# Performance work log

Measured on AMD Instinct MI355X. Metric: run time of the kernel, lower is better.

The kernel has to match this reference:

```python
import jax, jax.numpy as jnp
import numpy as np

B, L, H, NH, D, I = 2, 2048, 2048, 16, 128, 8192
EPS = 1e-6
ROPE_BASE = 10000.0


def rms_norm(x, w):
    x32 = x.astype(jnp.float32)
    n = x32 * jax.lax.rsqrt(jnp.mean(x32 * x32, axis=-1, keepdims=True) + EPS)
    return (n * w).astype(x.dtype)


def rope(x, offset):
    # x: [B, L, H, D], non-traditional (half-split) RoPE
    d = x.shape[-1]
    half = d // 2
    inv_freq = 1.0 / (ROPE_BASE ** (jnp.arange(half, dtype=jnp.float32) * 2.0 / d))
    pos = jnp.arange(x.shape[1], dtype=jnp.float32) + offset
    ang = pos[:, None] * inv_freq[None, :]              # [L, half]
    cos = jnp.cos(ang)[None, :, None, :]
    sin = jnp.sin(ang)[None, :, None, :]
    x1, x2 = x[..., :half], x[..., half:]
    out = jnp.concatenate([x1 * cos - x2 * sin, x2 * cos + x1 * sin], axis=-1)
    return out.astype(x.dtype)


def setup_inputs() -> dict:
    key = jax.random.key(0)
    ks = jax.random.split(key, 9)
    s = 0.02
    causal = jnp.where(jnp.tril(jnp.ones((L, L), dtype=bool)), 0.0, -1e9).astype(jnp.float32)
    return {
        "x": jax.random.normal(ks[0], (B, L, H), dtype=jnp.float32),
        "ln1_w": jnp.ones((H,), dtype=jnp.float32),
        "ln2_w": jnp.ones((H,), dtype=jnp.float32),
        "wq": jax.random.normal(ks[1], (H, H), dtype=jnp.float32) * s,
        "wk": jax.random.normal(ks[2], (H, H), dtype=jnp.float32) * s,
        "wv": jax.random.normal(ks[3], (H, H), dtype=jnp.float32) * s,
        "wo": jax.random.normal(ks[4], (H, H), dtype=jnp.float32) * s,
        "w_gate": jax.random.normal(ks[5], (I, H), dtype=jnp.float32) * s,
        "w_up": jax.random.normal(ks[6], (I, H), dtype=jnp.float32) * s,
        "w_down": jax.random.normal(ks[7], (H, I), dtype=jnp.float32) * s,
        "mask": causal,
        "offset": 0,
    }


def reference(x, ln1_w, ln2_w, wq, wk, wv, wo, w_gate, w_up, w_down, mask, offset):
    residual = x
    h = rms_norm(x, ln1_w)
    # QKV projections (torch Linear: y = x @ W.T)
    q = jnp.einsum("ble,oe->blo", h, wq).reshape(B, L, NH, D)
    k = jnp.einsum("ble,oe->blo", h, wk).reshape(B, L, NH, D)
    v = jnp.einsum("ble,oe->blo", h, wv).reshape(B, L, NH, D)
    q = rope(q, offset)
    k = rope(k, offset)
    # [B, NH, L, D]
    q = q.transpose(0, 2, 1, 3)
    k = k.transpose(0, 2, 1, 3)
    v = v.transpose(0, 2, 1, 3)
    scores = jnp.einsum("bhqd,bhkd->bhqk", q.astype(jnp.float32), k.astype(jnp.float32))
    scores = scores / np.sqrt(D).astype(np.float32)
    if mask is not None:
        scores = scores + mask
    probs = jax.nn.softmax(scores, axis=-1).astype(v.dtype)
    attn = jnp.einsum("bhqk,bhkd->bhqd", probs, v)
    attn = attn.transpose(0, 2, 1, 3).reshape(B, L, NH * D)
    h = jnp.einsum("blo,eo->ble", attn, wo)
    x = h + residual
    residual = x
    h = rms_norm(x, ln2_w)
    gate = jax.nn.silu(jnp.einsum("ble,ie->bli", h, w_gate))
    up = jnp.einsum("ble,ie->bli", h, w_up)
    mlp = jnp.einsum("bli,ei->ble", gate * up, w_down)
    return mlp + residual
```

## Files before the change

### kernel.cpp

```cpp
#include <hip/hip_runtime.h>
#include <stdint.h>

#define B_ 2
#define L_ 2048
#define H_ 2048
#define NH_ 16
#define D_ 128
#define I_ 8192
#define M_ (B_*L_)

typedef unsigned short u16;
typedef __attribute__((ext_vector_type(8))) short bf16x8;
typedef __attribute__((ext_vector_type(4))) float f32x4;

__device__ __forceinline__ u16 f2bf(float f) {
  union { float f; uint32_t u; } c; c.f = f;
  return (u16)((c.u + 0x7fffu + ((c.u >> 16) & 1u)) >> 16);
}
__device__ __forceinline__ float bf2f(u16 h) {
  union { uint32_t u; float f; } c; c.u = ((uint32_t)h) << 16;
  return c.f;
}
__device__ __forceinline__ void gload16(const void* g, void* l) {
  __builtin_amdgcn_global_load_lds(
      (__attribute__((address_space(1))) void*)g,
      (__attribute__((address_space(3))) void*)l, 16, 0, 0);
}

__global__ void cvt_w(const float* __restrict__ src, u16* __restrict__ dst, int n4) {
  int i = blockIdx.x * blockDim.x + threadIdx.x;
  if (i >= n4) return;
  float4 v = ((const float4*)src)[i];
  ushort4 o;
  o.x = f2bf(v.x); o.y = f2bf(v.y); o.z = f2bf(v.z); o.w = f2bf(v.w);
  ((ushort4*)dst)[i] = o;
}

__global__ __launch_bounds__(256) void down_reduce(const u16* __restrict__ p0,
                                                   const u16* __restrict__ p1,
                                                   const float* __restrict__ res,
                                                   float* __restrict__ out, int n4) {
  int i = blockIdx.x * blockDim.x + threadIdx.x;
  if (i >= n4) return;
  ushort4 a = ((const ushort4*)p0)[i];
  ushort4 b = ((const ushort4*)p1)[i];
  float4 r = ((const float4*)res)[i];
  float4 o;
  o.x = bf2f(a.x) + bf2f(b.x) + r.x;
  o.y = bf2f(a.y) + bf2f(b.y) + r.y;
  o.z = bf2f(a.z) + bf2f(b.z) + r.z;
  o.w = bf2f(a.w) + bf2f(b.w) + r.w;
  ((float4*)out)[i] = o;
}

__global__ __launch_bounds__(256) void rmsnorm_k(const float* __restrict__ x,
                                                 const float* __restrict__ w,
                                                 u16* __restrict__ out) {
  int row = blockIdx.x;
  int t = threadIdx.x;
  const float4* xr = (const float4*)(x + (size_t)row * H_);
  float4 a = xr[t * 2], b = xr[t * 2 + 1];
  float s = a.x*a.x + a.y*a.y + a.z*a.z + a.w*a.w
          + b.x*b.x + b.y*b.y + b.z*b.z + b.w*b.w;
  for (int m = 1; m < 64; m <<= 1) s += __shfl_xor(s, m);
  __shared__ float sm[4];
  if ((t & 63) == 0) sm[t >> 6] = s;
  __syncthreads();
  float tot = sm[0] + sm[1] + sm[2] + sm[3];
  float rs = rsqrtf(tot / (float)H_ + 1e-6f);
  const float4* wr = (const float4*)w;
  float4 w0 = wr[t * 2], w1 = wr[t * 2 + 1];
  ushort4 o0, o1;
  o0.x = f2bf(a.x * rs * w0.x); o0.y = f2bf(a.y * rs * w0.y);
  o0.z = f2bf(a.z * rs * w0.z); o0.w = f2bf(a.w * rs * w0.w);
  o1.x = f2bf(b.x * rs * w1.x); o1.y = f2bf(b.y * rs * w1.y);
  o1.z = f2bf(b.z * rs * w1.z); o1.w = f2bf(b.w * rs * w1.w);
  ushort4* orow = (ushort4*)(out + (size_t)row * H_);
  orow[t * 2] = o0; orow[t * 2 + 1] = o1;
}

__global__ void rope_tab(float* __restrict__ cosT, float* __restrict__ sinT,
                         const int* __restrict__ offp) {
  int i = blockIdx.x * blockDim.x + threadIdx.x;
  int d = i & 63, l = i >> 6;
  float inv = powf(10000.0f, -(float)d / 64.0f);
  float ang = (float)(l + *offp) * inv;
  cosT[i] = cosf(ang);
  sinT[i] = sinf(ang);
}

__global__ void rope_apply(u16* __restrict__ qk, const float* __restrict__ cosT,
                           const float* __restrict__ sinT) {
  int i = blockIdx.x * blockDim.x + threadIdx.x;
  int d = i & 63;
  size_t row = (size_t)(i >> 6);
  int l = (int)(row & (L_ - 1));
  u16* p = qk + row * D_;
  float x1 = bf2f(p[d]), x2 = bf2f(p[d + 64]);
  float c = cosT[l * 64 + d], s = sinT[l * 64 + d];
  p[d]      = f2bf(x1 * c - x2 * s);
  p[d + 64] = f2bf(x2 * c + x1 * s);
}

__global__ __launch_bounds__(256) void vtrans_k(const u16* __restrict__ v,
                                                u16* __restrict__ vt) {
  __shared__ u16 tile[64][65];
  int l0 = blockIdx.x * 64, d0 = blockIdx.y * 64;
  size_t base = (size_t)blockIdx.z * L_ * D_;
  int t = threadIdx.x;
  int tr = t >> 3, tc = (t & 7) * 8;
  #pragma unroll
  for (int it = 0; it < 2; ++it) {
    int r = tr + it * 32;
    const u16* src = v + base + (size_t)(l0 + r) * D_ + d0 + tc;
    ushort4 u0 = ((const ushort4*)src)[0], u1 = ((const ushort4*)src)[1];
    tile[r][tc + 0] = u0.x; tile[r][tc + 1] = u0.y;
    tile[r][tc + 2] = u0.z; tile[r][tc + 3] = u0.w;
    tile[r][tc + 4] = u1.x; tile[r][tc + 5] = u1.y;
    tile[r][tc + 6] = u1.z; tile[r][tc + 7] = u1.w;
  }
  __syncthreads();
  #pragma unroll
  for (int it = 0; it < 2; ++it) {
    int r = tr + it * 32;
    u16* dst = vt + base + (size_t)(d0 + r) * L_ + l0 + tc;
    ushort4 o0, o1;
    o0.x = tile[tc + 0][r]; o0.y = tile[tc + 1][r];
    o0.z = tile[tc + 2][r]; o0.w = tile[tc + 3][r];
    o1.x = tile[tc + 4][r]; o1.y = tile[tc + 5][r];
    o1.z = tile[tc + 6][r]; o1.w = tile[tc + 7][r];
    ((ushort4*)dst)[0] = o0; ((ushort4*)dst)[1] = o1;
  }
}

#define EPI_SILU 1
#define EPI_MUL 2
#define EPI_PART 4
#define EPI_QKV3 5

template <int EPI>
__global__ __launch_bounds__(512, 2)
void gemm256(const u16* __restrict__ A, const u16* __restrict__ Bw,
             int M, int N, int K, int nk,
             u16* __restrict__ outb, u16* __restrict__ outb2) {
  __shared__ __attribute__((aligned(16))) u16 Asm[2][2][8192];
  __shared__ __attribute__((aligned(16))) u16 Bsm[2][2][8192];
  int tid = threadIdx.x;
  int wid = tid >> 6, lane = tid & 63;
  int r16 = lane & 15, g4 = lane >> 4;
  int nwg = gridDim.x, bid = blockIdx.x;
  int q8 = nwg >> 3, r8 = nwg & 7, xcd = bid & 7, loc = bid >> 3;
  int wgall = (xcd < r8 ? xcd * (q8 + 1) : r8 * (q8 + 1) + (xcd - r8) * q8) + loc;
  int nwg_geo = (M >> 8) * (N >> 8);
  int ks = wgall / nwg_geo;
  int wg = wgall % nwg_geo;
  int MX = M >> 8;
  int m0 = (wg % MX) * 256;
  int n0 = (wg / MX) * 256;
  const char* Ab = (const char*)(A + (size_t)ks * nk * 64);
  const char* Bb = (const char*)(Bw + (size_t)ks * nk * 64);
  u16* ob = (EPI == EPI_PART && ks) ? outb2 : outb;

  f32x4 acc[2][2][4][2] = {};
  bf16x8 afr[4][2];
  bf16x8 bfr[2][2][2];

  auto STAGE = [&](int kt1, int sel) {
    if (kt1 >= nk) return;
    int buf = kt1 & 1;
    int k0 = kt1 << 6;
    const char* gb; char* lb; int row0;
    if (sel == 0)      { gb = Ab; row0 = m0;       lb = (char*)&Asm[buf][0][0]; }
    else if (sel == 3) { gb = Ab; row0 = m0 + 128; lb = (char*)&Asm[buf][1][0]; }
    else if (sel == 1) { gb = Bb; row0 = n0;       lb = (char*)&Bsm[buf][0][0]; }
    else               { gb = Bb; row0 = n0 + 128; lb = (char*)&Bsm[buf][1][0]; }
    #pragma unroll
    for (int j = 0; j < 2; ++j) {
      int p = j * 8192 + wid * 1024 + lane * 16;
      int r = p >> 7;
      int cb = (p & 127) ^ ((r & 7) << 4);
      gload16(gb + ((size_t)(row0 + r) * K + k0) * 2 + cb,
              lb + j * 8192 + wid * 1024);
    }
  };

  STAGE(0, 0); STAGE(0, 1); STAGE(0, 2); STAGE(0, 3);

  const int QM[4] = {0, 0, 1, 1};
  const int QN[4] = {0, 1, 1, 0};

  for (int kt = 0; kt < nk; ++kt) {
    int cur = kt & 1;
    #pragma unroll
    for (int ph = 0; ph < 4; ++ph) {
      if (ph < 3) {
        __builtin_amdgcn_sched_barrier(0);
        asm volatile("s_waitcnt vmcnt(4)" ::: "memory");
      }
      __builtin_amdgcn_s_barrier();
      __builtin_amdgcn_sched_barrier(0);
      const int qm = QM[ph], qn = QN[ph];
      if (ph == 0 || ph == 2) {
        const char* Ah = (const char*)&Asm[cur][qm][0];
        #pragma unroll
        for (int mf = 0; mf < 4; ++mf) {
          int R = (wid >> 2) * 64 + mf * 16 + r16;
          int sw = (R & 7) << 4;
          afr[mf][0] = *(const bf16x8*)(Ah + R * 128 + ((g4 * 16) ^ sw));
          afr[mf][1] = *(const bf16x8*)(Ah + R * 128 + ((64 + g4 * 16) ^ sw));
        }
      }
      if (ph == 0 || ph == 1) {
        const char* Bh = (const char*)&Bsm[cur][qn][0];
        #pragma unroll
        for (int nf = 0; nf < 2; ++nf) {
          int R = (wid & 3) * 32 + nf * 16 + r16;
          int sw = (R & 7) << 4;
          bfr[qn][nf][0] = *(const bf16x8*)(Bh + R * 128 + ((g4 * 16) ^ sw));
          bfr[qn][nf][1] = *(const bf16x8*)(Bh + R * 128 + ((64 + g4 * 16) ^ sw));
        }
      }
      STAGE(kt + 1, ph);
      __builtin_amdgcn_s_setprio(1);
      #pragma unroll
      for (int mf = 0; mf < 4; ++mf)
        #pragma unroll
        for (int nf = 0; nf < 2; ++nf)
          #pragma unroll
          for (int kk = 0; kk < 2; ++kk)
            acc[qm][qn][mf][nf] = __builtin_amdgcn_mfma_f32_16x16x32_bf16(
                afr[mf][kk], bfr[qn][nf][kk], acc[qm][qn][mf][nf], 0, 0, 0);
      __builtin_amdgcn_s_setprio(0);
    }
  }
  #pragma unroll
  for (int qm = 0; qm < 2; ++qm)
    #pragma unroll
    for (int qn = 0; qn < 2; ++qn)
      #pragma unroll
      for (int mf = 0; mf < 4; ++mf)
        #pragma unroll
        for (int nf = 0; nf < 2; ++nf)
          #pragma unroll
          for (int rr = 0; rr < 4; ++rr) {
            int row = m0 + qm * 128 + (wid >> 2) * 64 + mf * 16 + g4 * 4 + rr;
            int col = n0 + qn * 128 + (wid & 3) * 32 + nf * 16 + r16;
            float val = acc[qm][qn][mf][nf][rr];
            if (EPI == EPI_SILU) {
              ob[(size_t)row * N + col] = f2bf(val / (1.0f + __expf(-val)));
            } else if (EPI == EPI_MUL) {
              float g = bf2f(ob[(size_t)row * N + col]);
              ob[(size_t)row * N + col] = f2bf(g * val);
            } else if (EPI == EPI_PART) {
              ob[(size_t)row * N + col] = f2bf(val);
            } else if (EPI == EPI_QKV3) {
              int which = col >> 11, within = col & 2047;
              int hh = within >> 7, d = within & 127;
              int bb = row >> 11, l = row & 2047;
              ob[(size_t)which * M_ * H_ +
                 ((((size_t)bb * NH_ + hh) * L_ + l) << 7) + d] = f2bf(val);
            }
          }
}

__global__ __launch_bounds__(256)
void flash_attn(const u16* __restrict__ q, const u16* __restrict__ k,
                const u16* __restrict__ vt, u16* __restrict__ out) {
  __shared__ __attribute__((aligned(16))) u16 Kt[2][64 * 128];
  __shared__ __attribute__((aligned(16))) u16 Vt[2][128 * 64];
  __shared__ __attribute__((aligned(16))) u16 Pl[4][16 * 64];
  int tid = threadIdx.x, w = tid >> 6, lane = tid & 63;
  int r16 = lane & 15, g4 = lane >> 4;
  int b = blockIdx.z, h = blockIdx.y;
  int qt = gridDim.x - 1 - blockIdx.x;
  int q0 = qt * 64;
  size_t bh = (size_t)b * NH_ + h;
  const char* qb = (const char*)(q + bh * L_ * D_);
  const char* kb = (const char*)(k + bh * L_ * D_);
  const char* vb = (const char*)(vt + bh * D_ * L_);
  int qrow = q0 + w * 16 + r16;
  bf16x8 qf[4];
  #pragma unroll
  for (int c = 0; c < 4; ++c)
    qf[c] = *(const bf16x8*)(qb + ((size_t)qrow * 128 + c * 32 + g4 * 8) * 2);
  f32x4 oacc[8] = {};
  float mrow[4], lsum[4];
  #pragma unroll
  for (int r = 0; r < 4; ++r) { mrow[r] = -3.0e38f; lsum[r] = 0.f; }
  int myq = q0 + w * 16 + g4 * 4;
  int ntiles = qt + 1;
  int rsw = (r16 & 7) << 4;
  const float sc = 0.08838834764831845f;

  auto STAGEKV = [&](int t, int buf) {
    if (t >= ntiles) return;
    int kv0 = t * 64;
    #pragma unroll
    for (int i = 0; i < 4; ++i) {
      int uoff = i * 4096 + w * 1024;
      int lin = uoff + lane * 16;
      int krow = lin >> 8;
      int kcol = (lin & 255) ^ ((krow & 7) << 4);
      gload16(kb + (size_t)(kv0 + krow) * 256 + kcol,
              (char*)&Kt[buf][0] + uoff);
      int vrow = lin >> 7;
      int vcol = (lin & 127) ^ ((vrow & 7) << 4);
      gload16(vb + (size_t)vrow * (L_ * 2) + kv0 * 2 + vcol,
              (char*)&Vt[buf][0] + uoff);
    }
  };

  STAGEKV(0, 0);
  __syncthreads();

  for (int t = 0; t < ntiles; ++t) {
    int buf = t & 1;
    int kv0 = t * 64;
    STAGEKV(t + 1, buf ^ 1);
    const char* Kb = (const char*)&Kt[buf][0];
    const char* Vb = (const char*)&Vt[buf][0];
    f32x4 s[4] = {};
    __builtin_amdgcn_s_setprio(1);
    #pragma unroll
    for (int c = 0; c < 4; ++c) {
      #pragma unroll
      for (int n = 0; n < 4; ++n) {
        bf16x8 kf = *(const bf16x8*)(Kb + (n * 16 + r16) * 256
                                     + ((c * 64 + g4 * 16) ^ rsw));
        s[n] = __builtin_amdgcn_mfma_f32_16x16x32_bf16(qf[c], kf, s[n], 0, 0, 0);
      }
    }
    __builtin_amdgcn_s_setprio(0);
    #pragma unroll
    for (int r = 0; r < 4; ++r) {
      float rm = -3.0e38f;
      #pragma unroll
      for (int n = 0; n < 4; ++n) {
        float v = s[n][r] * sc;
        int kvi = kv0 + n * 16 + r16;
        if (kvi > myq + r) v = -3.0e38f;
        s[n][r] = v;
        rm = fmaxf(rm, v);
      }
      rm = fmaxf(rm, __shfl_xor(rm, 1));
      rm = fmaxf(rm, __shfl_xor(rm, 2));
      rm = fmaxf(rm, __shfl_xor(rm, 4));
      rm = fmaxf(rm, __shfl_xor(rm, 8));
      float mnew = fmaxf(mrow[r], rm);
      float alpha = __expf(mrow[r] - mnew);
      mrow[r] = mnew;
      lsum[r] *= alpha;
      #pragma unroll
      for (int nf = 0; nf < 8; ++nf) oacc[nf][r] *= alpha;
      int prow = g4 * 4 + r;
      int psw = (prow & 7) << 3;
      #pragma unroll
      for (int n = 0; n < 4; ++n) {
        float pv = __expf(s[n][r] - mnew);
        lsum[r] += pv;
        Pl[w][prow * 64 + ((n * 16 + r16) ^ psw)] = f2bf(pv);
      }
    }
    asm volatile("s_waitcnt lgkmcnt(0)" ::: "memory");
    __builtin_amdgcn_sched_barrier(0);
    __builtin_amdgcn_s_setprio(1);
    #pragma unroll
    for (int kc = 0; kc < 2; ++kc) {
      bf16x8 pf = *(const bf16x8*)((const char*)&Pl[w][0] + r16 * 128
                                   + ((kc * 64 + g4 * 16) ^ rsw));
      #pragma unroll
      for (int nf = 0; nf < 8; ++nf) {
        bf16x8 vf = *(const bf16x8*)(Vb + (nf * 16 + r16) * 128
                                     + ((kc * 64 + g4 * 16) ^ rsw));
        oacc[nf] = __builtin_amdgcn_mfma_f32_16x16x32_bf16(pf, vf, oacc[nf], 0, 0, 0);
      }
    }
    __builtin_amdgcn_s_setprio(0);
    __syncthreads();
  }
  #pragma unroll
  for (int r = 0; r < 4; ++r) {
    float l = lsum[r];
    l += __shfl_xor(l, 1); l += __shfl_xor(l, 2);
    l += __shfl_xor(l, 4); l += __shfl_xor(l, 8);
    float inv = 1.0f / l;
    size_t orow = ((size_t)b * L_ + (myq + r)) * H_ + h * D_;
    #pragma unroll
    for (int nf = 0; nf < 8; ++nf)
      out[orow + nf * 16 + r16] = f2bf(oacc[nf][r] * inv);
  }
}

extern "C" void kernel_launch(void* const* d_in, const int* in_sizes, int n_in,
                              void* d_out, int out_size, void* d_ws, size_t ws_size,
                              hipStream_t stream) {
  (void)in_sizes; (void)n_in; (void)out_size; (void)ws_size;
  const float* x    = (const float*)d_in[0];
  const float* ln1w = (const float*)d_in[1];
  const float* ln2w = (const float*)d_in[2];
  const float* wq   = (const float*)d_in[3];
  const float* wk   = (const float*)d_in[4];
  const float* wv   = (const float*)d_in[5];
  const float* wo   = (const float*)d_in[6];
  const float* wg   = (const float*)d_in[7];
  const float* wu   = (const float*)d_in[8];
  const float* wd   = (const float*)d_in[9];
  const int*   offp = (const int*)d_in[11];
  float* out = (float*)d_out;

  char* p = (char*)d_ws;
  auto alloc = [&](size_t bytes) {
    char* r = p;
    p += (bytes + 255) & ~(size_t)255;
    return r;
  };
  const size_t HH = (size_t)H_ * H_, IH = (size_t)I_ * H_;
  u16* wbuf = (u16*)alloc(IH * 2);
  u16* h1   = (u16*)alloc((size_t)M_ * H_ * 2);
  u16* qb   = (u16*)alloc((size_t)M_ * H_ * 2);
  u16* kb   = (u16*)alloc((size_t)M_ * H_ * 2);
  u16* vb   = (u16*)alloc((size_t)M_ * H_ * 2);
  u16* vtb  = (u16*)alloc((size_t)M_ * H_ * 2);
  u16* attn = (u16*)alloc((size_t)M_ * H_ * 2);
  float* x2 = (float*)alloc((size_t)M_ * H_ * 4);
  float* cosT = (float*)alloc((size_t)L_ * 64 * 4);
  float* sinT = (float*)alloc((size_t)L_ * 64 * 4);
  u16* h2    = h1;
  u16* gateb = qb;

  const int nHH4 = (int)(HH / 4), nIH4 = (int)(IH / 4);

  rmsnorm_k<<<M_, 256, 0, stream>>>(x, ln1w, h1);
  rope_tab<<<(L_ * 64) / 256, 256, 0, stream>>>(cosT, sinT, offp);

  cvt_w<<<nHH4 / 256, 256, 0, stream>>>(wq, wbuf, nHH4);
  cvt_w<<<nHH4 / 256, 256, 0, stream>>>(wk, wbuf + HH, nHH4);
  cvt_w<<<nHH4 / 256, 256, 0, stream>>>(wv, wbuf + 2 * HH, nHH4);
  int nwg_qkv = (M_ / 256) * (3 * H_ / 256);
  gemm256<EPI_QKV3><<<nwg_qkv, 512, 0, stream>>>(h1, wbuf, M_, 3 * H_, H_,
                                                 H_ / 64, qb, nullptr);

  int nrope = B_ * NH_ * L_ * 64;
  rope_apply<<<nrope / 256, 256, 0, stream>>>(qb, cosT, sinT);
  rope_apply<<<nrope / 256, 256, 0, stream>>>(qb + (size_t)M_ * H_, cosT, sinT);
  vtrans_k<<<dim3(L_ / 64, D_ / 64, B_ * NH_), 256, 0, stream>>>(
      qb + 2 * (size_t)M_ * H_, vtb);

  flash_attn<<<dim3(L_ / 64, NH_, B_), 256, 0, stream>>>(
      qb, qb + (size_t)M_ * H_, vtb, attn);

  cvt_w<<<nHH4 / 256, 256, 0, stream>>>(wo, wbuf, nHH4);
  int nwg_wo = 2 * (M_ / 256) * (H_ / 256);
  gemm256<EPI_PART><<<nwg_wo, 512, 0, stream>>>(attn, wbuf, M_, H_, H_,
                                                H_ / 128, kb, vb);
  down_reduce<<<(M_ * H_ / 4) / 256, 256, 0, stream>>>(kb, vb, x, x2,
                                                       M_ * H_ / 4);
  rmsnorm_k<<<M_, 256, 0, stream>>>(x2, ln2w, h2);

  int nwg256 = (M_ / 256) * (I_ / 256);
  cvt_w<<<nIH4 / 256, 256, 0, stream>>>(wg, wbuf, nIH4);
  gemm256<EPI_SILU><<<nwg256, 512, 0, stream>>>(h2, wbuf, M_, I_, H_,
                                                H_ / 64, gateb, nullptr);
  cvt_w<<<nIH4 / 256, 256, 0, stream>>>(wu, wbuf, nIH4);
  gemm256<EPI_MUL><<<nwg256, 512, 0, stream>>>(h2, wbuf, M_, I_, H_,
                                               H_ / 64, gateb, nullptr);

  cvt_w<<<nIH4 / 256, 256, 0, stream>>>(wd, wbuf, nIH4);
  int nwg_dn = 2 * (M_ / 256) * (H_ / 256);
  gemm256<EPI_PART><<<nwg_dn, 512, 0, stream>>>(gateb, wbuf, M_, H_, I_,
                                                I_ / 128, h1, attn);
  down_reduce<<<(M_ * H_ / 4) / 256, 256, 0, stream>>>(h1, attn, x2, out,
                                                       M_ * H_ / 4);
}
```

Before: 852.4 us.

## Fuse gate/up GEMMs into one GLU kernel and widen attention query tiles

Adds an EPI_GLU mode in which each workgroup stages matching 128-column slices of the gate and up weights into the two B halves. The SiLU(gate)*up product is computed in registers, which removes the read-modify-write of the gate buffer and a second pass over the activations. The fused path depends on extra workspace for a second converted weight copy and falls back to the old two-GEMM path otherwise. Flash attention now processes 128 query rows per block (two 16-row fragments per wave), so each staged K/V tile is reused by twice as many rows. The cost is more registers and a doubled P buffer, which may lower occupancy.

```diff
diff --git a/kernel.cpp b/kernel.cpp
--- a/kernel.cpp
+++ b/kernel.cpp
@@ -137,12 +137,14 @@
 #define EPI_MUL 2
 #define EPI_PART 4
 #define EPI_QKV3 5
+#define EPI_GLU 6
 
 template <int EPI>
 __global__ __launch_bounds__(512, 2)
 void gemm256(const u16* __restrict__ A, const u16* __restrict__ Bw,
              int M, int N, int K, int nk,
-             u16* __restrict__ outb, u16* __restrict__ outb2) {
+             u16* __restrict__ outb, u16* __restrict__ outb2,
+             const u16* __restrict__ Bw2) {
   __shared__ __attribute__((aligned(16))) u16 Asm[2][2][8192];
   __shared__ __attribute__((aligned(16))) u16 Bsm[2][2][8192];
   int tid = threadIdx.x;
@@ -151,14 +153,15 @@
   int nwg = gridDim.x, bid = blockIdx.x;
   int q8 = nwg >> 3, r8 = nwg & 7, xcd = bid & 7, loc = bid >> 3;
   int wgall = (xcd < r8 ? xcd * (q8 + 1) : r8 * (q8 + 1) + (xcd - r8) * q8) + loc;
-  int nwg_geo = (M >> 8) * (N >> 8);
+  int nwg_geo = (M >> 8) * ((EPI == EPI_GLU) ? (N >> 7) : (N >> 8));
   int ks = wgall / nwg_geo;
   int wg = wgall % nwg_geo;
   int MX = M >> 8;
   int m0 = (wg % MX) * 256;
-  int n0 = (wg / MX) * 256;
+  int n0 = (wg / MX) * ((EPI == EPI_GLU) ? 128 : 256);
   const char* Ab = (const char*)(A + (size_t)ks * nk * 64);
   const char* Bb = (const char*)(Bw + (size_t)ks * nk * 64);
+  const char* Bb2 = (const char*)Bw2;
   u16* ob = (EPI == EPI_PART && ks) ? outb2 : outb;
 
   f32x4 acc[2][2][4][2] = {};
@@ -173,7 +176,9 @@
     if (sel == 0)      { gb = Ab; row0 = m0;       lb = (char*)&Asm[buf][0][0]; }
     else if (sel == 3) { gb = Ab; row0 = m0 + 128; lb = (char*)&Asm[buf][1][0]; }
     else if (sel == 1) { gb = Bb; row0 = n0;       lb = (char*)&Bsm[buf][0][0]; }
-    else               { gb = Bb; row0 = n0 + 128; lb = (char*)&Bsm[buf][1][0]; }
+    else               { gb = (EPI == EPI_GLU) ? Bb2 : Bb;
+                         row0 = (EPI == EPI_GLU) ? n0 : n0 + 128;
+                         lb = (char*)&Bsm[buf][1][0]; }
     #pragma unroll
     for (int j = 0; j < 2; ++j) {
       int p = j * 8192 + wid * 1024 + lane * 16;
@@ -232,6 +237,24 @@
                 afr[mf][kk], bfr[qn][nf][kk], acc[qm][qn][mf][nf], 0, 0, 0);
       __builtin_amdgcn_s_setprio(0);
     }
+  }
+  if (EPI == EPI_GLU) {
+    #pragma unroll
+    for (int qm = 0; qm < 2; ++qm)
+      #pragma unroll
+      for (int mf = 0; mf < 4; ++mf)
+        #pragma unroll
+        for (int nf = 0; nf < 2; ++nf)
+          #pragma unroll
+          for (int rr = 0; rr < 4; ++rr) {
+            int row = m0 + qm * 128 + (wid >> 2) * 64 + mf * 16 + g4 * 4 + rr;
+            int col = n0 + (wid & 3) * 32 + nf * 16 + r16;
+            float g = acc[qm][0][mf][nf][rr];
+            float u = acc[qm][1][mf][nf][rr];
+            float sg = g / (1.0f + __expf(-g));
+            outb[(size_t)row * N + col] = f2bf(sg * u);
+          }
+    return;
   }
   #pragma unroll
   for (int qm = 0; qm < 2; ++qm)
@@ -268,27 +291,32 @@
                 const u16* __restrict__ vt, u16* __restrict__ out) {
   __shared__ __attribute__((aligned(16))) u16 Kt[2][64 * 128];
   __shared__ __attribute__((aligned(16))) u16 Vt[2][128 * 64];
-  __shared__ __attribute__((aligned(16))) u16 Pl[4][16 * 64];
+  __shared__ __attribute__((aligned(16))) u16 Pl[4][32 * 64];
   int tid = threadIdx.x, w = tid >> 6, lane = tid & 63;
   int r16 = lane & 15, g4 = lane >> 4;
   int b = blockIdx.z, h = blockIdx.y;
   int qt = gridDim.x - 1 - blockIdx.x;
-  int q0 = qt * 64;
+  int q0 = qt * 128;
   size_t bh = (size_t)b * NH_ + h;
   const char* qb = (const char*)(q + bh * L_ * D_);
   const char* kb = (const char*)(k + bh * L_ * D_);
   const char* vb = (const char*)(vt + bh * D_ * L_);
-  int qrow = q0 + w * 16 + r16;
-  bf16x8 qf[4];
+  bf16x8 qf[2][4];
   #pragma unroll
-  for (int c = 0; c < 4; ++c)
-    qf[c] = *(const bf16x8*)(qb + ((size_t)qrow * 128 + c * 32 + g4 * 8) * 2);
-  f32x4 oacc[8] = {};
-  float mrow[4], lsum[4];
+  for (int rf = 0; rf < 2; ++rf) {
+    int qrow = q0 + w * 32 + rf * 16 + r16;
+    #pragma unroll
+    for (int c = 0; c < 4; ++c)
+      qf[rf][c] = *(const bf16x8*)(qb + ((size_t)qrow * 128 + c * 32 + g4 * 8) * 2);
+  }
+  f32x4 oacc[2][8] = {};
+  float mrow[2][4], lsum[2][4];
   #pragma unroll
-  for (int r = 0; r < 4; ++r) { mrow[r] = -3.0e38f; lsum[r] = 0.f; }
-  int myq = q0 + w * 16 + g4 * 4;
-  int ntiles = qt + 1;
+  for (int rf = 0; rf < 2; ++rf)
+    #pragma unroll
+    for (int r = 0; r < 4; ++r) { mrow[rf][r] = -3.0e38f; lsum[rf][r] = 0.f; }
+  int myq0 = q0 + w * 32 + g4 * 4;
+  int ntiles = 2 * qt + 2;
   int rsw = (r16 & 7) << 4;
   const float sc = 0.08838834764831845f;
 
@@ -319,7 +347,7 @@
     STAGEKV(t + 1, buf ^ 1);
     const char* Kb = (const char*)&Kt[buf][0];
     const char* Vb = (const char*)&Vt[buf][0];
-    f32x4 s[4] = {};
+    f32x4 s[2][4] = {};
     __builtin_amdgcn_s_setprio(1);
     #pragma unroll
     for (int c = 0; c < 4; ++c) {
@@ -327,38 +355,43 @@
       for (int n = 0; n < 4; ++n) {
         bf16x8 kf = *(const bf16x8*)(Kb + (n * 16 + r16) * 256
                                      + ((c * 64 + g4 * 16) ^ rsw));
-        s[n] = __builtin_amdgcn_mfma_f32_16x16x32_bf16(qf[c], kf, s[n], 0, 0, 0);
+        s[0][n] = __builtin_amdgcn_mfma_f32_16x16x32_bf16(qf[0][c], kf, s[0][n], 0, 0, 0);
+        s[1][n] = __builtin_amdgcn_mfma_f32_16x16x32_bf16(qf[1][c], kf, s[1][n], 0, 0, 0);
       }
     }
     __builtin_amdgcn_s_setprio(0);
     #pragma unroll
-    for (int r = 0; r < 4; ++r) {
-      float rm = -3.0e38f;
-      #pragma unroll
-      for (int n = 0; n < 4; ++n) {
-        float v = s[n][r] * sc;
-        int kvi = kv0 + n * 16 + r16;
-        if (kvi > myq + r) v = -3.0e38f;
-        s[n][r] = v;
-        rm = fmaxf(rm, v);
-      }
-      rm = fmaxf(rm, __shfl_xor(rm, 1));
-      rm = fmaxf(rm, __shfl_xor(rm, 2));
-      rm = fmaxf(rm, __shfl_xor(rm, 4));
-      rm = fmaxf(rm, __shfl_xor(rm, 8));
-      float mnew = fmaxf(mrow[r], rm);
-      float alpha = __expf(mrow[r] - mnew);
-      mrow[r] = mnew;
-      lsum[r] *= alpha;
-      #pragma unroll
-      for (int nf = 0; nf < 8; ++nf) oacc[nf][r] *= alpha;
-      int prow = g4 * 4 + r;
-      int psw = (prow & 7) << 3;
-      #pragma unroll
-      for (int n = 0; n < 4; ++n) {
-        float pv = __expf(s[n][r] - mnew);
-        lsum[r] += pv;
-        Pl[w][prow * 64 + ((n * 16 + r16) ^ psw)] = f2bf(pv);
+    for (int rf = 0; rf < 2; ++rf) {
+      int myq = myq0 + rf * 16;
+      #pragma unroll
+      for (int r = 0; r < 4; ++r) {
+        float rm = -3.0e38f;
+        #pragma unroll
+        for (int n = 0; n < 4; ++n) {
+          float v = s[rf][n][r] * sc;
+          int kvi = kv0 + n * 16 + r16;
+          if (kvi > myq + r) v = -3.0e38f;
+          s[rf][n][r] = v;
+          rm = fmaxf(rm, v);
+        }
+        rm = fmaxf(rm, __shfl_xor(rm, 1));
+        rm = fmaxf(rm, __shfl_xor(rm, 2));
+        rm = fmaxf(rm, __shfl_xor(rm, 4));
+        rm = fmaxf(rm, __shfl_xor(rm, 8));
+        float mnew = fmaxf(mrow[rf][r], rm);
+        float alpha = __expf(mrow[rf][r] - mnew);
+        mrow[rf][r] = mnew;
+        lsum[rf][r] *= alpha;
+        #pragma unroll
+        for (int nf = 0; nf < 8; ++nf) oacc[rf][nf][r] *= alpha;
+        int prow = rf * 16 + g4 * 4 + r;
+        int psw = (prow & 7) << 3;
+        #pragma unroll
+        for (int n = 0; n < 4; ++n) {
+          float pv = __expf(s[rf][n][r] - mnew);
+          lsum[rf][r] += pv;
+          Pl[w][prow * 64 + ((n * 16 + r16) ^ psw)] = f2bf(pv);
+        }
       }
     }
     asm volatile("s_waitcnt lgkmcnt(0)" ::: "memory");
@@ -366,35 +399,41 @@
     __builtin_amdgcn_s_setprio(1);
     #pragma unroll
     for (int kc = 0; kc < 2; ++kc) {
-      bf16x8 pf = *(const bf16x8*)((const char*)&Pl[w][0] + r16 * 128
-                                   + ((kc * 64 + g4 * 16) ^ rsw));
+      bf16x8 pf0 = *(const bf16x8*)((const char*)&Pl[w][0] + r16 * 128
+                                    + ((kc * 64 + g4 * 16) ^ rsw));
+      bf16x8 pf1 = *(const bf16x8*)((const char*)&Pl[w][0] + (16 + r16) * 128
+                                    + ((kc * 64 + g4 * 16) ^ rsw));
       #pragma unroll
       for (int nf = 0; nf < 8; ++nf) {
         bf16x8 vf = *(const bf16x8*)(Vb + (nf * 16 + r16) * 128
                                      + ((kc * 64 + g4 * 16) ^ rsw));
-        oacc[nf] = __builtin_amdgcn_mfma_f32_16x16x32_bf16(pf, vf, oacc[nf], 0, 0, 0);
+        oacc[0][nf] = __builtin_amdgcn_mfma_f32_16x16x32_bf16(pf0, vf, oacc[0][nf], 0, 0, 0);
+        oacc[1][nf] = __builtin_amdgcn_mfma_f32_16x16x32_bf16(pf1, vf, oacc[1][nf], 0, 0, 0);
       }
     }
     __builtin_amdgcn_s_setprio(0);
     __syncthreads();
   }
   #pragma unroll
-  for (int r = 0; r < 4; ++r) {
-    float l = lsum[r];
-    l += __shfl_xor(l, 1); l += __shfl_xor(l, 2);
-    l += __shfl_xor(l, 4); l += __shfl_xor(l, 8);
-    float inv = 1.0f / l;
-    size_t orow = ((size_t)b * L_ + (myq + r)) * H_ + h * D_;
-    #pragma unroll
-    for (int nf = 0; nf < 8; ++nf)
-      out[orow + nf * 16 + r16] = f2bf(oacc[nf][r] * inv);
+  for (int rf = 0; rf < 2; ++rf) {
+    #pragma unroll
+    for (int r = 0; r < 4; ++r) {
+      float l = lsum[rf][r];
+      l += __shfl_xor(l, 1); l += __shfl_xor(l, 2);
+      l += __shfl_xor(l, 4); l += __shfl_xor(l, 8);
+      float inv = 1.0f / l;
+      size_t orow = ((size_t)b * L_ + (myq0 + rf * 16 + r)) * H_ + h * D_;
+      #pragma unroll
+      for (int nf = 0; nf < 8; ++nf)
+        out[orow + nf * 16 + r16] = f2bf(oacc[rf][nf][r] * inv);
+    }
   }
 }
 
 extern "C" void kernel_launch(void* const* d_in, const int* in_sizes, int n_in,
                               void* d_out, int out_size, void* d_ws, size_t ws_size,
                               hipStream_t stream) {
-  (void)in_sizes; (void)n_in; (void)out_size; (void)ws_size;
+  (void)in_sizes; (void)n_in; (void)out_size;
   const float* x    = (const float*)d_in[0];
   const float* ln1w = (const float*)d_in[1];
   const float* ln2w = (const float*)d_in[2];
@@ -427,6 +466,8 @@
   float* sinT = (float*)alloc((size_t)L_ * 64 * 4);
   u16* h2    = h1;
   u16* gateb = qb;
+  u16* wu_b = (u16*)alloc(IH * 2);
+  bool fused_glu = ((char*)wu_b + IH * 2) <= ((char*)d_ws + ws_size);
 
   const int nHH4 = (int)(HH / 4), nIH4 = (int)(IH / 4);
 
@@ -438,7 +479,7 @@
   cvt_w<<<nHH4 / 256, 256, 0, stream>>>(wv, wbuf + 2 * HH, nHH4);
   int nwg_qkv = (M_ / 256) * (3 * H_ / 256);
   gemm256<EPI_QKV3><<<nwg_qkv, 512, 0, stream>>>(h1, wbuf, M_, 3 * H_, H_,
-                                                 H_ / 64, qb, nullptr);
+                                                 H_ / 64, qb, nullptr, nullptr);
 
   int nrope = B_ * NH_ * L_ * 64;
   rope_apply<<<nrope / 256, 256, 0, stream>>>(qb, cosT, sinT);
@@ -446,29 +487,37 @@
   vtrans_k<<<dim3(L_ / 64, D_ / 64, B_ * NH_), 256, 0, stream>>>(
       qb + 2 * (size_t)M_ * H_, vtb);
 
-  flash_attn<<<dim3(L_ / 64, NH_, B_), 256, 0, stream>>>(
+  flash_attn<<<dim3(L_ / 128, NH_, B_), 256, 0, stream>>>(
       qb, qb + (size_t)M_ * H_, vtb, attn);
 
   cvt_w<<<nHH4 / 256, 256, 0, stream>>>(wo, wbuf, nHH4);
   int nwg_wo = 2 * (M_ / 256) * (H_ / 256);
   gemm256<EPI_PART><<<nwg_wo, 512, 0, stream>>>(attn, wbuf, M_, H_, H_,
-                                                H_ / 128, kb, vb);
+                                                H_ / 128, kb, vb, nullptr);
   down_reduce<<<(M_ * H_ / 4) / 256, 256, 0, stream>>>(kb, vb, x, x2,
                                                        M_ * H_ / 4);
   rmsnorm_k<<<M_, 256, 0, stream>>>(x2, ln2w, h2);
 
-  int nwg256 = (M_ / 256) * (I_ / 256);
-  cvt_w<<<nIH4 / 256, 256, 0, stream>>>(wg, wbuf, nIH4);
-  gemm256<EPI_SILU><<<nwg256, 512, 0, stream>>>(h2, wbuf, M_, I_, H_,
-                                                H_ / 64, gateb, nullptr);
-  cvt_w<<<nIH4 / 256, 256, 0, stream>>>(wu, wbuf, nIH4);
-  gemm256<EPI_MUL><<<nwg256, 512, 0, stream>>>(h2, wbuf, M_, I_, H_,
-                                               H_ / 64, gateb, nullptr);
+  if (fused_glu) {
+    cvt_w<<<nIH4 / 256, 256, 0, stream>>>(wg, wbuf, nIH4);
+    cvt_w<<<nIH4 / 256, 256, 0, stream>>>(wu, wu_b, nIH4);
+    int nwg_glu = (M_ / 256) * (I_ / 128);
+    gemm256<EPI_GLU><<<nwg_glu, 512, 0, stream>>>(h2, wbuf, M_, I_, H_,
+                                                  H_ / 64, gateb, nullptr, wu_b);
+  } else {
+    int nwg256 = (M_ / 256) * (I_ / 256);
+    cvt_w<<<nIH4 / 256, 256, 0, stream>>>(wg, wbuf, nIH4);
+    gemm256<EPI_SILU><<<nwg256, 512, 0, stream>>>(h2, wbuf, M_, I_, H_,
+                                                  H_ / 64, gateb, nullptr, nullptr);
+    cvt_w<<<nIH4 / 256, 256, 0, stream>>>(wu, wbuf, nIH4);
+    gemm256<EPI_MUL><<<nwg256, 512, 0, stream>>>(h2, wbuf, M_, I_, H_,
+                                                 H_ / 64, gateb, nullptr, nullptr);
+  }
 
   cvt_w<<<nIH4 / 256, 256, 0, stream>>>(wd, wbuf, nIH4);
   int nwg_dn = 2 * (M_ / 256) * (H_ / 256);
   gemm256<EPI_PART><<<nwg_dn, 512, 0, stream>>>(gateb, wbuf, M_, H_, I_,
-                                                I_ / 128, h1, attn);
+                                                I_ / 128, h1, attn, nullptr);
   down_reduce<<<(M_ * H_ / 4) / 256, 256, 0, stream>>>(h1, attn, x2, out,
                                                        M_ * H_ / 4);
 }
```

After: 832.9 us. 1.02x faster.

## Fuse gate and up projections into one GEMM with SiLU-multiply epilogue

Applied to the files above, without the earlier changes.

Adds an EPI_GLU variant of the 256-wide GEMM in which each workgroup loads a 128-column slice of the gate weights and the same slice of the up weights into its two B halves. It computes both products for a 256x128 output tile and writes silu(gate)*up directly. This drops the intermediate gate write and read-back, and it removes the second pass over the normalized activations. It needs a second bf16 weight buffer in the workspace and keeps the old two-GEMM path as a fallback when the workspace is too small.

```diff
diff --git a/kernel.cpp b/kernel.cpp
--- a/kernel.cpp
+++ b/kernel.cpp
@@ -137,12 +137,14 @@
 #define EPI_MUL 2
 #define EPI_PART 4
 #define EPI_QKV3 5
+#define EPI_GLU 6
 
 template <int EPI>
 __global__ __launch_bounds__(512, 2)
 void gemm256(const u16* __restrict__ A, const u16* __restrict__ Bw,
              int M, int N, int K, int nk,
-             u16* __restrict__ outb, u16* __restrict__ outb2) {
+             u16* __restrict__ outb, u16* __restrict__ outb2,
+             const u16* __restrict__ Bw2) {
   __shared__ __attribute__((aligned(16))) u16 Asm[2][2][8192];
   __shared__ __attribute__((aligned(16))) u16 Bsm[2][2][8192];
   int tid = threadIdx.x;
@@ -151,14 +153,15 @@
   int nwg = gridDim.x, bid = blockIdx.x;
   int q8 = nwg >> 3, r8 = nwg & 7, xcd = bid & 7, loc = bid >> 3;
   int wgall = (xcd < r8 ? xcd * (q8 + 1) : r8 * (q8 + 1) + (xcd - r8) * q8) + loc;
-  int nwg_geo = (M >> 8) * (N >> 8);
+  int nwg_geo = (M >> 8) * ((EPI == EPI_GLU) ? (N >> 7) : (N >> 8));
   int ks = wgall / nwg_geo;
   int wg = wgall % nwg_geo;
   int MX = M >> 8;
   int m0 = (wg % MX) * 256;
-  int n0 = (wg / MX) * 256;
+  int n0 = (wg / MX) * ((EPI == EPI_GLU) ? 128 : 256);
   const char* Ab = (const char*)(A + (size_t)ks * nk * 64);
   const char* Bb = (const char*)(Bw + (size_t)ks * nk * 64);
+  const char* Bb2 = (const char*)Bw2;
   u16* ob = (EPI == EPI_PART && ks) ? outb2 : outb;
 
   f32x4 acc[2][2][4][2] = {};
@@ -173,7 +176,9 @@
     if (sel == 0)      { gb = Ab; row0 = m0;       lb = (char*)&Asm[buf][0][0]; }
     else if (sel == 3) { gb = Ab; row0 = m0 + 128; lb = (char*)&Asm[buf][1][0]; }
     else if (sel == 1) { gb = Bb; row0 = n0;       lb = (char*)&Bsm[buf][0][0]; }
-    else               { gb = Bb; row0 = n0 + 128; lb = (char*)&Bsm[buf][1][0]; }
+    else               { gb = (EPI == EPI_GLU) ? Bb2 : Bb;
+                         row0 = (EPI == EPI_GLU) ? n0 : n0 + 128;
+                         lb = (char*)&Bsm[buf][1][0]; }
     #pragma unroll
     for (int j = 0; j < 2; ++j) {
       int p = j * 8192 + wid * 1024 + lane * 16;
@@ -232,6 +237,24 @@
                 afr[mf][kk], bfr[qn][nf][kk], acc[qm][qn][mf][nf], 0, 0, 0);
       __builtin_amdgcn_s_setprio(0);
     }
+  }
+  if (EPI == EPI_GLU) {
+    #pragma unroll
+    for (int qm = 0; qm < 2; ++qm)
+      #pragma unroll
+      for (int mf = 0; mf < 4; ++mf)
+        #pragma unroll
+        for (int nf = 0; nf < 2; ++nf)
+          #pragma unroll
+          for (int rr = 0; rr < 4; ++rr) {
+            int row = m0 + qm * 128 + (wid >> 2) * 64 + mf * 16 + g4 * 4 + rr;
+            int col = n0 + (wid & 3) * 32 + nf * 16 + r16;
+            float g = acc[qm][0][mf][nf][rr];
+            float u = acc[qm][1][mf][nf][rr];
+            float sg = g / (1.0f + __expf(-g));
+            outb[(size_t)row * N + col] = f2bf(sg * u);
+          }
+    return;
   }
   #pragma unroll
   for (int qm = 0; qm < 2; ++qm)
@@ -394,7 +417,7 @@
 extern "C" void kernel_launch(void* const* d_in, const int* in_sizes, int n_in,
                               void* d_out, int out_size, void* d_ws, size_t ws_size,
                               hipStream_t stream) {
-  (void)in_sizes; (void)n_in; (void)out_size; (void)ws_size;
+  (void)in_sizes; (void)n_in; (void)out_size;
   const float* x    = (const float*)d_in[0];
   const float* ln1w = (const float*)d_in[1];
   const float* ln2w = (const float*)d_in[2];
@@ -427,6 +450,8 @@
   float* sinT = (float*)alloc((size_t)L_ * 64 * 4);
   u16* h2    = h1;
   u16* gateb = qb;
+  u16* wu_b = (u16*)alloc(IH * 2);
+  bool fused_glu = ((char*)wu_b + IH * 2) <= ((char*)d_ws + ws_size);
 
   const int nHH4 = (int)(HH / 4), nIH4 = (int)(IH / 4);
 
@@ -438,7 +463,7 @@
   cvt_w<<<nHH4 / 256, 256, 0, stream>>>(wv, wbuf + 2 * HH, nHH4);
   int nwg_qkv = (M_ / 256) * (3 * H_ / 256);
   gemm256<EPI_QKV3><<<nwg_qkv, 512, 0, stream>>>(h1, wbuf, M_, 3 * H_, H_,
-                                                 H_ / 64, qb, nullptr);
+                                                 H_ / 64, qb, nullptr, nullptr);
 
   int nrope = B_ * NH_ * L_ * 64;
   rope_apply<<<nrope / 256, 256, 0, stream>>>(qb, cosT, sinT);
@@ -452,23 +477,31 @@
   cvt_w<<<nHH4 / 256, 256, 0, stream>>>(wo, wbuf, nHH4);
   int nwg_wo = 2 * (M_ / 256) * (H_ / 256);
   gemm256<EPI_PART><<<nwg_wo, 512, 0, stream>>>(attn, wbuf, M_, H_, H_,
-                                                H_ / 128, kb, vb);
+                                                H_ / 128, kb, vb, nullptr);
   down_reduce<<<(M_ * H_ / 4) / 256, 256, 0, stream>>>(kb, vb, x, x2,
                                                        M_ * H_ / 4);
   rmsnorm_k<<<M_, 256, 0, stream>>>(x2, ln2w, h2);
 
-  int nwg256 = (M_ / 256) * (I_ / 256);
-  cvt_w<<<nIH4 / 256, 256, 0, stream>>>(wg, wbuf, nIH4);
-  gemm256<EPI_SILU><<<nwg256, 512, 0, stream>>>(h2, wbuf, M_, I_, H_,
-                                                H_ / 64, gateb, nullptr);
-  cvt_w<<<nIH4 / 256, 256, 0, stream>>>(wu, wbuf, nIH4);
-  gemm256<EPI_MUL><<<nwg256, 512, 0, stream>>>(h2, wbuf, M_, I_, H_,
-                                               H_ / 64, gateb, nullptr);
+  if (fused_glu) {
+    cvt_w<<<nIH4 / 256, 256, 0, stream>>>(wg, wbuf, nIH4);
+    cvt_w<<<nIH4 / 256, 256, 0, stream>>>(wu, wu_b, nIH4);
+    int nwg_glu = (M_ / 256) * (I_ / 128);
+    gemm256<EPI_GLU><<<nwg_glu, 512, 0, stream>>>(h2, wbuf, M_, I_, H_,
+                                                  H_ / 64, gateb, nullptr, wu_b);
+  } else {
+    int nwg256 = (M_ / 256) * (I_ / 256);
+    cvt_w<<<nIH4 / 256, 256, 0, stream>>>(wg, wbuf, nIH4);
+    gemm256<EPI_SILU><<<nwg256, 512, 0, stream>>>(h2, wbuf, M_, I_, H_,
+                                                  H_ / 64, gateb, nullptr, nullptr);
+    cvt_w<<<nIH4 / 256, 256, 0, stream>>>(wu, wbuf, nIH4);
+    gemm256<EPI_MUL><<<nwg256, 512, 0, stream>>>(h2, wbuf, M_, I_, H_,
+                                                 H_ / 64, gateb, nullptr, nullptr);
+  }
 
   cvt_w<<<nIH4 / 256, 256, 0, stream>>>(wd, wbuf, nIH4);
   int nwg_dn = 2 * (M_ / 256) * (H_ / 256);
   gemm256<EPI_PART><<<nwg_dn, 512, 0, stream>>>(gateb, wbuf, M_, H_, I_,
-                                                I_ / 128, h1, attn);
+                                                I_ / 128, h1, attn, nullptr);
   down_reduce<<<(M_ * H_ / 4) / 256, 256, 0, stream>>>(h1, attn, x2, out,
                                                        M_ * H_ / 4);
 }
```

Result: faster. 794.7 us (-6.8%).
